# Optimization experiments

Measured on AMD Instinct MI355X. Metric: run time of the kernel, lower is better.

## Reference

```python
import jax, jax.numpy as jnp
import numpy as np

EPS = 1e-5  # BatchNorm eps


def _spmm(x, src, dst, dinv, n):
    # normalized adjacency SpMM: out[d] = dinv[d] * sum_{(s,d) in E} dinv[s] * x[s]
    msg = x[src] * dinv[src][:, None]                      # [E, d]
    agg = jax.ops.segment_sum(msg, dst, num_segments=n)   # [N, d]
    return agg * dinv[:, None]


def _cheb(x, W, b, src, dst, dinv, n):
    # Chebyshev recursion with lambda_max=2: Lhat = -Ahat
    # T0 = X, T1 = Lhat X, Tk = 2 Lhat T_{k-1} - T_{k-2}; out = sum_k T_k W_k + b
    X0 = x
    X1 = -_spmm(x, src, dst, dinv, n)
    out = X0 @ W[0] + X1 @ W[1]
    Xp, Xc = X0, X1
    for k in range(2, W.shape[0]):
        Xn = -2.0 * _spmm(Xc, src, dst, dinv, n) - Xp
        out = out + Xn @ W[k]
        Xp, Xc = Xc, Xn
    return out + b


def _bn(x, gamma, beta):
    # BatchNorm1d over nodes (training-mode batch stats)
    mu = jnp.mean(x, axis=0)
    var = jnp.var(x, axis=0)
    return (x - mu) * jax.lax.rsqrt(var + EPS) * gamma + beta


def setup_inputs() -> dict:
    key = jax.random.key(0)
    ks = jax.random.split(key, 8)
    n, e, fin, h, fout, K = 50000, 800000, 128, 128, 64, 3
    def w(k, shape, fan_in):
        return jax.random.normal(k, shape, jnp.float32) * np.float32(1.0 / np.sqrt(fan_in))
    return {
        "features": jax.random.normal(ks[0], (n, fin), jnp.float32),
        "src": jax.random.randint(ks[1], (e,), 0, n),
        "dst": jax.random.randint(ks[2], (e,), 0, n),
        "W1": w(ks[3], (K, fin, h), K * fin), "b1": jnp.zeros((h,), jnp.float32),
        "W2": w(ks[4], (K, h, h), K * h), "b2": jnp.zeros((h,), jnp.float32),
        "W3": w(ks[5], (K, h, h), K * h), "b3": jnp.zeros((h,), jnp.float32),
        "gamma": jnp.ones((h,), jnp.float32), "beta": jnp.zeros((h,), jnp.float32),
        "mw1": w(ks[6], (h, h), h), "mb1": jnp.zeros((h,), jnp.float32),
        "mw2": w(ks[7], (h, fout), h), "mb2": jnp.zeros((fout,), jnp.float32),
    }


def reference(features, src, dst, W1, b1, W2, b2, W3, b3, gamma, beta, mw1, mb1, mw2, mb2):
    n = features.shape[0]
    deg = jax.ops.segment_sum(jnp.ones(dst.shape, features.dtype), dst, num_segments=n)
    dinv = jax.lax.rsqrt(jnp.maximum(deg, 1.0))
    x = jax.nn.relu(_cheb(features, W1, b1, src, dst, dinv, n))
    x = _bn(x, gamma, beta)
    for _ in range(1, 3):  # self.k = 3 -> cheb2 applied twice (shared weights)
        x = jax.nn.relu(_cheb(x, W2, b2, src, dst, dinv, n))
    x_res = x
    x = jax.nn.relu(_cheb(x, W3, b3, src, dst, dinv, n))
    x = x + x_res  # dropout treated as identity (eval mode)
    return jax.nn.relu(x @ mw1 + mb1) @ mw2 + mb2
```

## Files before the change

kernel.cpp:

```cpp
#include <hip/hip_runtime.h>
#include <hip/hip_bf16.h>

typedef __attribute__((ext_vector_type(4))) float f32x4;
typedef __attribute__((ext_vector_type(8))) short short8;

__device__ inline unsigned short f2bf(float f) {
    union { float f; unsigned int u; } v; v.f = f;
    unsigned int u = v.u;
    return (unsigned short)((u + 0x7fffu + ((u >> 16) & 1u)) >> 16);
}
__device__ inline float bf2f(unsigned short h) {
    union { unsigned int u; float f; } v; v.u = ((unsigned int)h) << 16; return v.f;
}
__device__ inline float bflo(unsigned int p) {
    union { unsigned int u; float f; } v; v.u = p << 16; return v.f;
}
__device__ inline float bfhi(unsigned int p) {
    union { unsigned int u; float f; } v; v.u = p & 0xffff0000u; return v.f;
}
__device__ inline unsigned int packbf(float a, float b) {
    return (unsigned int)f2bf(a) | ((unsigned int)f2bf(b) << 16);
}


__global__ __launch_bounds__(256) void cast_k(const float* __restrict__ x, unsigned short* __restrict__ y, int n4) {
    int i = blockIdx.x * 256 + threadIdx.x;
    if (i >= n4) return;
    f32x4 v = ((const f32x4*)x)[i];
    uint2 o; o.x = packbf(v[0], v[1]); o.y = packbf(v[2], v[3]);
    ((uint2*)y)[i] = o;
}


__global__ __launch_bounds__(256) void deg_count_k(const int* __restrict__ dst, int* __restrict__ deg, int e) {
    int i = blockIdx.x * 256 + threadIdx.x;
    if (i < e) atomicAdd(&deg[dst[i]], 1);
}

__global__ __launch_bounds__(256) void partial_k(const int* __restrict__ deg, int* __restrict__ part, int n) {
    __shared__ int sm[256];
    int t = threadIdx.x;
    int base = blockIdx.x * 1024 + t * 4;
    int s = 0;
#pragma unroll
    for (int j = 0; j < 4; ++j) { int idx = base + j; if (idx < n) s += deg[idx]; }
    sm[t] = s;
    __syncthreads();
    for (int off = 128; off > 0; off >>= 1) {
        if (t < off) sm[t] += sm[t + off];
        __syncthreads();
    }
    if (t == 0) part[blockIdx.x] = sm[0];
}

__global__ __launch_bounds__(256) void scanpart_k(int* __restrict__ part, int nb) {
    __shared__ int sm[256];
    int t = threadIdx.x;
    int v = (t < nb) ? part[t] : 0;
    sm[t] = v;
    __syncthreads();
    for (int off = 1; off < 256; off <<= 1) {
        int u = (t >= off) ? sm[t - off] : 0;
        __syncthreads();
        sm[t] += u;
        __syncthreads();
    }
    if (t < nb) part[t] = sm[t] - v;
}

__global__ __launch_bounds__(256) void rowptr_k(const int* __restrict__ deg, const int* __restrict__ part,
                                                int* __restrict__ rowptr, int* __restrict__ cursor,
                                                float* __restrict__ dinv, int n) {
    __shared__ int sm[256];
    int t = threadIdx.x;
    int base = blockIdx.x * 1024 + t * 4;
    int d[4]; int s = 0;
#pragma unroll
    for (int j = 0; j < 4; ++j) { int idx = base + j; d[j] = (idx < n) ? deg[idx] : 0; s += d[j]; }
    sm[t] = s;
    __syncthreads();
    for (int off = 1; off < 256; off <<= 1) {
        int u = (t >= off) ? sm[t - off] : 0;
        __syncthreads();
        sm[t] += u;
        __syncthreads();
    }
    int ex = part[blockIdx.x] + sm[t] - s;
#pragma unroll
    for (int j = 0; j < 4; ++j) {
        int idx = base + j;
        if (idx < n) {
            rowptr[idx] = ex; cursor[idx] = ex;
            dinv[idx] = rsqrtf(fmaxf((float)d[j], 1.0f));
        }
        ex += d[j];
    }
    if (blockIdx.x == gridDim.x - 1 && t == 255) rowptr[n] = part[blockIdx.x] + sm[255];
}

__global__ __launch_bounds__(256) void scatter_k(const int* __restrict__ src, const int* __restrict__ dst,
                                                 int* __restrict__ cursor, int* __restrict__ csrc, int e) {
    int i = blockIdx.x * 256 + threadIdx.x;
    if (i < e) {
        int p = atomicAdd(&cursor[dst[i]], 1);
        csrc[p] = src[i];
    }
}


__global__ __launch_bounds__(256) void spmm_bf_k(const unsigned short* __restrict__ x, const int* __restrict__ rowptr,
                                                 const int* __restrict__ csrc, const float* __restrict__ dinv,
                                                 unsigned short* __restrict__ out, int n) {
    int lane = threadIdx.x & 63;
    int wave = threadIdx.x >> 6;
    int node = blockIdx.x * 4 + wave;
    if (node >= n) return;
    int g = lane >> 4;
    int c = lane & 15;
    int beg = rowptr[node], end = rowptr[node + 1];
    float acc[8];
#pragma unroll
    for (int j = 0; j < 8; ++j) acc[j] = 0.f;

    int i = beg + g;
    for (; i + 12 < end; i += 16) {
        int s0 = csrc[i], s1 = csrc[i + 4], s2 = csrc[i + 8], s3 = csrc[i + 12];
        float w0 = dinv[s0], w1 = dinv[s1], w2 = dinv[s2], w3 = dinv[s3];
        uint4 v0 = ((const uint4*)(x + (size_t)s0 * 128))[c];
        uint4 v1 = ((const uint4*)(x + (size_t)s1 * 128))[c];
        uint4 v2 = ((const uint4*)(x + (size_t)s2 * 128))[c];
        uint4 v3 = ((const uint4*)(x + (size_t)s3 * 128))[c];
        acc[0] += w0 * bflo(v0.x); acc[1] += w0 * bfhi(v0.x);
        acc[2] += w0 * bflo(v0.y); acc[3] += w0 * bfhi(v0.y);
        acc[4] += w0 * bflo(v0.z); acc[5] += w0 * bfhi(v0.z);
        acc[6] += w0 * bflo(v0.w); acc[7] += w0 * bfhi(v0.w);
        acc[0] += w1 * bflo(v1.x); acc[1] += w1 * bfhi(v1.x);
        acc[2] += w1 * bflo(v1.y); acc[3] += w1 * bfhi(v1.y);
        acc[4] += w1 * bflo(v1.z); acc[5] += w1 * bfhi(v1.z);
        acc[6] += w1 * bflo(v1.w); acc[7] += w1 * bfhi(v1.w);
        acc[0] += w2 * bflo(v2.x); acc[1] += w2 * bfhi(v2.x);
        acc[2] += w2 * bflo(v2.y); acc[3] += w2 * bfhi(v2.y);
        acc[4] += w2 * bflo(v2.z); acc[5] += w2 * bfhi(v2.z);
        acc[6] += w2 * bflo(v2.w); acc[7] += w2 * bfhi(v2.w);
        acc[0] += w3 * bflo(v3.x); acc[1] += w3 * bfhi(v3.x);
        acc[2] += w3 * bflo(v3.y); acc[3] += w3 * bfhi(v3.y);
        acc[4] += w3 * bflo(v3.z); acc[5] += w3 * bfhi(v3.z);
        acc[6] += w3 * bflo(v3.w); acc[7] += w3 * bfhi(v3.w);
    }
    for (; i < end; i += 4) {
        int s0 = csrc[i];
        float w0 = dinv[s0];
        uint4 v0 = ((const uint4*)(x + (size_t)s0 * 128))[c];
        acc[0] += w0 * bflo(v0.x); acc[1] += w0 * bfhi(v0.x);
        acc[2] += w0 * bflo(v0.y); acc[3] += w0 * bfhi(v0.y);
        acc[4] += w0 * bflo(v0.z); acc[5] += w0 * bfhi(v0.z);
        acc[6] += w0 * bflo(v0.w); acc[7] += w0 * bfhi(v0.w);
    }

#pragma unroll
    for (int j = 0; j < 8; ++j) {
        acc[j] += __shfl_xor(acc[j], 16, 64);
        acc[j] += __shfl_xor(acc[j], 32, 64);
    }

    float dd = dinv[node];
    if (g == 0) {
        uint4 o;
        o.x = packbf(acc[0] * dd, acc[1] * dd);
        o.y = packbf(acc[2] * dd, acc[3] * dd);
        o.z = packbf(acc[4] * dd, acc[5] * dd);
        o.w = packbf(acc[6] * dd, acc[7] * dd);
        ((uint4*)(out + (size_t)node * 128))[c] = o;
    }
}


__global__ __launch_bounds__(256) void pack_w_k(const float* __restrict__ W, unsigned short* __restrict__ out,
                                                int K, int N, int cheb) {
    int id = blockIdx.x * 256 + threadIdx.x;
    int total = (K / 32) * (N / 16) * 64;
    if (id >= total) return;
    int lane = id & 63;
    int t2 = id >> 6;
    int nf = N / 16;
    int f = t2 % nf;
    int ks = t2 / nf;
    int col = f * 16 + (lane & 15);
    int kbase = ks * 32 + ((lane >> 4) * 8);
    for (int j = 0; j < 8; ++j) {
        int kg = kbase + j;
        float v;
        if (cheb) {
            int t = kg >> 7, kk = kg & 127;
            const float* W0 = W;
            const float* Wb = W + 16384;
            const float* Wc = W + 32768;
            float w0 = W0[kk * 128 + col], wb = Wb[kk * 128 + col], wc = Wc[kk * 128 + col];
            v = (t == 0) ? (w0 - wc) : (t == 1) ? (-wb) : (2.0f * wc);
        } else {
            v = W[(size_t)kg * N + col];
        }
        out[(size_t)id * 8 + j] = f2bf(v);
    }
}


template<int KSTEPS, int NF, bool RELU, bool RES, bool OUTF32>
__global__ __launch_bounds__(256) void gemm_k(const unsigned short* __restrict__ s0,
                                              const unsigned short* __restrict__ s1,
                                              const unsigned short* __restrict__ s2,
                                              const unsigned short* __restrict__ wp,
                                              const float* __restrict__ bias,
                                              const unsigned short* __restrict__ resid,
                                              void* __restrict__ outv, int n) {
    int lane = threadIdx.x & 63;
    int wave = threadIdx.x >> 6;
    int row0 = blockIdx.x * 64 + wave * 16;
    if (row0 >= n) return;
    int rowA = row0 + (lane & 15);
    if (rowA >= n) rowA = n - 1;
    int kg = (lane >> 4) * 8;

    f32x4 acc[NF];
#pragma unroll
    for (int f = 0; f < NF; ++f) acc[f] = (f32x4)(0.0f);

#pragma unroll
    for (int ks = 0; ks < KSTEPS; ++ks) {
        const unsigned short* sp;
        int kk;
        if (KSTEPS == 12) {
            sp = (ks < 4) ? s0 : ((ks < 8) ? s1 : s2);
            kk = (ks & 3) * 32 + kg;
        } else {
            sp = s0;
            kk = ks * 32 + kg;
        }
        short8 a = *(const short8*)(sp + (size_t)rowA * 128 + kk);
#pragma unroll
        for (int f = 0; f < NF; ++f) {
            short8 b = *(const short8*)(wp + ((size_t)(ks * NF + f) * 512 + lane * 8));
            acc[f] = __builtin_amdgcn_mfma_f32_16x16x32_bf16(a, b, acc[f], 0, 0, 0);
        }
    }

    int colb = lane & 15;
    int rowD = row0 + ((lane >> 4) << 2);
#pragma unroll
    for (int f = 0; f < NF; ++f) {
        int c = f * 16 + colb;
        float bv = bias[c];
#pragma unroll
        for (int r = 0; r < 4; ++r) {
            int row = rowD + r;
            if (row >= n) continue;
            float v = acc[f][r] + bv;
            if (RELU) v = fmaxf(v, 0.0f);
            if (RES) v += bf2f(resid[(size_t)row * 128 + c]);
            if (OUTF32) ((float*)outv)[(size_t)row * (NF * 16) + c] = v;
            else        ((unsigned short*)outv)[(size_t)row * (NF * 16) + c] = f2bf(v);
        }
    }
}


__global__ __launch_bounds__(256) void mlp_fused_k(const unsigned short* __restrict__ x,
                                                   const unsigned short* __restrict__ wp1,
                                                   const float* __restrict__ mb1,
                                                   const unsigned short* __restrict__ wp2,
                                                   const float* __restrict__ mb2,
                                                   float* __restrict__ out, int n) {
    __shared__ unsigned short tlds[64 * 128];
    int lane = threadIdx.x & 63;
    int wave = threadIdx.x >> 6;
    int row0 = blockIdx.x * 64 + wave * 16;
    int rowA = row0 + (lane & 15);
    if (rowA >= n) rowA = n - 1;
    int kg = (lane >> 4) * 8;
    int colb = lane & 15;

    f32x4 acc[8];
#pragma unroll
    for (int f = 0; f < 8; ++f) acc[f] = (f32x4)(0.0f);
#pragma unroll
    for (int ks = 0; ks < 4; ++ks) {
        short8 a = *(const short8*)(x + (size_t)rowA * 128 + ks * 32 + kg);
#pragma unroll
        for (int f = 0; f < 8; ++f) {
            short8 b = *(const short8*)(wp1 + ((size_t)(ks * 8 + f) * 512 + lane * 8));
            acc[f] = __builtin_amdgcn_mfma_f32_16x16x32_bf16(a, b, acc[f], 0, 0, 0);
        }
    }
    int lrowD = wave * 16 + ((lane >> 4) << 2);
#pragma unroll
    for (int f = 0; f < 8; ++f) {
        int c = f * 16 + colb;
        float bv = mb1[c];
#pragma unroll
        for (int r = 0; r < 4; ++r) {
            int lrow = lrowD + r;
            float v = fmaxf(acc[f][r] + bv, 0.0f);
            int byte = lrow * 256 + c * 2;
            byte ^= ((lrow & 7) << 4);
            *(unsigned short*)((char*)tlds + byte) = f2bf(v);
        }
    }
    __syncthreads();

    f32x4 acc2[4];
#pragma unroll
    for (int f = 0; f < 4; ++f) acc2[f] = (f32x4)(0.0f);
    int lrowA = wave * 16 + (lane & 15);
#pragma unroll
    for (int ks = 0; ks < 4; ++ks) {
        int byte = lrowA * 256 + (ks * 32 + kg) * 2;
        byte ^= ((lrowA & 7) << 4);
        short8 a = *(const short8*)((const char*)tlds + byte);
#pragma unroll
        for (int f = 0; f < 4; ++f) {
            short8 b = *(const short8*)(wp2 + ((size_t)(ks * 4 + f) * 512 + lane * 8));
            acc2[f] = __builtin_amdgcn_mfma_f32_16x16x32_bf16(a, b, acc2[f], 0, 0, 0);
        }
    }
    int rowD = row0 + ((lane >> 4) << 2);
#pragma unroll
    for (int f = 0; f < 4; ++f) {
        int c = f * 16 + colb;
        float bv = mb2[c];
#pragma unroll
        for (int r = 0; r < 4; ++r) {
            int row = rowD + r;
            if (row >= n) continue;
            out[(size_t)row * 64 + c] = acc2[f][r] + bv;
        }
    }
}


__global__ __launch_bounds__(256) void bn_stats_k(const unsigned short* __restrict__ x, float* __restrict__ gsum,
                                                  float* __restrict__ gsqs, int n) {
    __shared__ float s1[256], s2[256];
    int c = threadIdx.x & 127;
    int h = threadIdx.x >> 7;
    int r0 = blockIdx.x * 256;
    int rend = r0 + 256; if (rend > n) rend = n;
    float a = 0.f, b = 0.f;
    for (int r = r0 + h; r < rend; r += 2) {
        float v = bf2f(x[(size_t)r * 128 + c]);
        a += v; b += v * v;
    }
    s1[threadIdx.x] = a; s2[threadIdx.x] = b;
    __syncthreads();
    if (threadIdx.x < 128) {
        a = s1[threadIdx.x] + s1[threadIdx.x + 128];
        b = s2[threadIdx.x] + s2[threadIdx.x + 128];
        atomicAdd(&gsum[c], a);
        atomicAdd(&gsqs[c], b);
    }
}

__global__ __launch_bounds__(256) void bn_apply_k(unsigned short* __restrict__ x, const float* __restrict__ gsum,
                                                  const float* __restrict__ gsqs, const float* __restrict__ gamma,
                                                  const float* __restrict__ beta, int n, float inv_n) {
    int i = blockIdx.x * 256 + threadIdx.x;
    if (i >= n * 32) return;
    int c4 = (i & 31) * 4;
    uint2 p = ((uint2*)x)[i];
    float f[4] = { bflo(p.x), bfhi(p.x), bflo(p.y), bfhi(p.y) };
#pragma unroll
    for (int j = 0; j < 4; ++j) {
        int c = c4 + j;
        float mu = gsum[c] * inv_n;
        float var = gsqs[c] * inv_n - mu * mu;
        float sc = rsqrtf(var + 1e-5f) * gamma[c];
        f[j] = (f[j] - mu) * sc + beta[c];
    }
    p.x = packbf(f[0], f[1]);
    p.y = packbf(f[2], f[3]);
    ((uint2*)x)[i] = p;
}


extern "C" void kernel_launch(void* const* d_in, const int* in_sizes, int n_in,
                              void* d_out, int out_size, void* d_ws, size_t ws_size,
                              hipStream_t stream) {
    const float* feat  = (const float*)d_in[0];
    const int*   src   = (const int*)d_in[1];
    const int*   dst   = (const int*)d_in[2];
    const float* W1    = (const float*)d_in[3];
    const float* b1    = (const float*)d_in[4];
    const float* W2    = (const float*)d_in[5];
    const float* b2    = (const float*)d_in[6];
    const float* W3    = (const float*)d_in[7];
    const float* b3    = (const float*)d_in[8];
    const float* gamma = (const float*)d_in[9];
    const float* beta  = (const float*)d_in[10];
    const float* mw1   = (const float*)d_in[11];
    const float* mb1   = (const float*)d_in[12];
    const float* mw2   = (const float*)d_in[13];
    const float* mb2   = (const float*)d_in[14];
    float* outp = (float*)d_out;

    const int n = in_sizes[0] / 128;
    const int e = in_sizes[1];

    char* w = (char*)d_ws;
    auto alloc = [&](size_t bytes) -> void* {
        void* p = (void*)w;
        w += (bytes + 255) & ~(size_t)255;
        return p;
    };
    unsigned short* featb = (unsigned short*)alloc((size_t)n * 128 * 2);
    unsigned short* buf0  = (unsigned short*)alloc((size_t)n * 128 * 2);
    unsigned short* buf1  = (unsigned short*)alloc((size_t)n * 128 * 2);
    unsigned short* buf2  = (unsigned short*)alloc((size_t)n * 128 * 2);
    unsigned short* buf3  = (unsigned short*)alloc((size_t)n * 128 * 2);
    int*   deg    = (int*)alloc((size_t)n * 4);
    float* dinv   = (float*)alloc((size_t)n * 4);
    int*   rowptr = (int*)alloc((size_t)(n + 1) * 4);
    int*   cursor = (int*)alloc((size_t)n * 4);
    int*   csrc   = (int*)alloc((size_t)e * 4);
    int*   part   = (int*)alloc(256 * 4);
    unsigned short* wp1  = (unsigned short*)alloc(12 * 8 * 512 * 2);
    unsigned short* wp2  = (unsigned short*)alloc(12 * 8 * 512 * 2);
    unsigned short* wp3  = (unsigned short*)alloc(12 * 8 * 512 * 2);
    unsigned short* wpm1 = (unsigned short*)alloc(4 * 8 * 512 * 2);
    unsigned short* wpm2 = (unsigned short*)alloc(4 * 4 * 512 * 2);
    float* gsum = (float*)alloc(128 * 4);
    float* gsqs = (float*)alloc(128 * 4);

    const int gE = (e + 255) / 256;
    const int gGemm = (n + 63) / 64;
    const int gSpmm = (n + 3) / 4;
    const int gBnS = (n + 255) / 256;
    const int gBnA = (n * 32 + 255) / 256;
    const int nb = (n + 1023) / 1024;

    cast_k<<<(n * 32 + 255) / 256, 256, 0, stream>>>(feat, featb, n * 32);

    hipMemsetAsync(deg, 0, (size_t)n * 4, stream);
    deg_count_k<<<gE, 256, 0, stream>>>(dst, deg, e);
    partial_k<<<nb, 256, 0, stream>>>(deg, part, n);
    scanpart_k<<<1, 256, 0, stream>>>(part, nb);
    rowptr_k<<<nb, 256, 0, stream>>>(deg, part, rowptr, cursor, dinv, n);
    scatter_k<<<gE, 256, 0, stream>>>(src, dst, cursor, csrc, e);

    pack_w_k<<<(12 * 8 * 64 + 255) / 256, 256, 0, stream>>>(W1, wp1, 384, 128, 1);
    pack_w_k<<<(12 * 8 * 64 + 255) / 256, 256, 0, stream>>>(W2, wp2, 384, 128, 1);
    pack_w_k<<<(12 * 8 * 64 + 255) / 256, 256, 0, stream>>>(W3, wp3, 384, 128, 1);
    pack_w_k<<<(4 * 8 * 64 + 255) / 256, 256, 0, stream>>>(mw1, wpm1, 128, 128, 0);
    pack_w_k<<<(4 * 4 * 64 + 255) / 256, 256, 0, stream>>>(mw2, wpm2, 128, 64, 0);

    spmm_bf_k<<<gSpmm, 256, 0, stream>>>(featb, rowptr, csrc, dinv, buf1, n);
    spmm_bf_k<<<gSpmm, 256, 0, stream>>>(buf1, rowptr, csrc, dinv, buf2, n);
    gemm_k<12, 8, true, false, false><<<gGemm, 256, 0, stream>>>(featb, buf1, buf2, wp1, b1, nullptr, buf0, n);

    hipMemsetAsync(gsum, 0, 128 * 4, stream);
    hipMemsetAsync(gsqs, 0, 128 * 4, stream);
    bn_stats_k<<<gBnS, 256, 0, stream>>>(buf0, gsum, gsqs, n);
    bn_apply_k<<<gBnA, 256, 0, stream>>>(buf0, gsum, gsqs, gamma, beta, n, 1.0f / (float)n);

    spmm_bf_k<<<gSpmm, 256, 0, stream>>>(buf0, rowptr, csrc, dinv, buf1, n);
    spmm_bf_k<<<gSpmm, 256, 0, stream>>>(buf1, rowptr, csrc, dinv, buf2, n);
    gemm_k<12, 8, true, false, false><<<gGemm, 256, 0, stream>>>(buf0, buf1, buf2, wp2, b2, nullptr, buf3, n);

    spmm_bf_k<<<gSpmm, 256, 0, stream>>>(buf3, rowptr, csrc, dinv, buf1, n);
    spmm_bf_k<<<gSpmm, 256, 0, stream>>>(buf1, rowptr, csrc, dinv, buf2, n);
    gemm_k<12, 8, true, false, false><<<gGemm, 256, 0, stream>>>(buf3, buf1, buf2, wp2, b2, nullptr, buf0, n);

    spmm_bf_k<<<gSpmm, 256, 0, stream>>>(buf0, rowptr, csrc, dinv, buf1, n);
    spmm_bf_k<<<gSpmm, 256, 0, stream>>>(buf1, rowptr, csrc, dinv, buf2, n);
    gemm_k<12, 8, true, true, false><<<gGemm, 256, 0, stream>>>(buf0, buf1, buf2, wp3, b3, buf0, buf3, n);

    mlp_fused_k<<<gGemm, 256, 0, stream>>>(buf3, wpm1, mb1, wpm2, mb2, outp, n);
}
```

Before: 540.3 us.

## Fuse BN stats into GEMM, fold BN affine into SpMM, partition atomics by dst range

BatchNorm statistics are now gathered in the first Chebyshev GEMM epilogue through shared-memory atomics, and a tiny kernel turns them into scale and offset. The BN affine is no longer applied in a separate pass. It is folded into the next SpMM, using the sum of neighbour weights for the offset term, and into the GEMM A-operand load for the T0 slice. Degree counting and CSR scatter now split destination nodes into 8 ranges so concurrent atomics land in a smaller address window, at the cost of reading dst 8 times. The five weight-pack launches are merged into one. Together these remove two full passes over the activations and several launches, while adding per-element affine arithmetic in the GEMM inner loop.

```diff
diff --git a/kernel.cpp b/kernel.cpp
--- a/kernel.cpp
+++ b/kernel.cpp
@@ -21,6 +21,8 @@
 __device__ inline unsigned int packbf(float a, float b) {
     return (unsigned int)f2bf(a) | ((unsigned int)f2bf(b) << 16);
 }
+
+#define EPT 4096
 
 
 __global__ __launch_bounds__(256) void cast_k(const float* __restrict__ x, unsigned short* __restrict__ y, int n4) {
@@ -32,9 +34,18 @@
 }
 
 
-__global__ __launch_bounds__(256) void deg_count_k(const int* __restrict__ dst, int* __restrict__ deg, int e) {
-    int i = blockIdx.x * 256 + threadIdx.x;
-    if (i < e) atomicAdd(&deg[dst[i]], 1);
+__global__ __launch_bounds__(256) void deg_count8_k(const int* __restrict__ dst, int* __restrict__ deg,
+                                                    int e, int n, int n8) {
+    int r = blockIdx.x & 7;
+    int chunk = blockIdx.x >> 3;
+    int base = chunk * EPT;
+    int lim = base + EPT; if (lim > e) lim = e;
+    int lo = r * n8;
+    int hi = lo + n8; if (hi > n) hi = n;
+    for (int i = base + threadIdx.x; i < lim; i += 256) {
+        int d = dst[i];
+        if (d >= lo && d < hi) atomicAdd(&deg[d], 1);
+    }
 }
 
 __global__ __launch_bounds__(256) void partial_k(const int* __restrict__ deg, int* __restrict__ part, int n) {
@@ -98,18 +109,29 @@
     if (blockIdx.x == gridDim.x - 1 && t == 255) rowptr[n] = part[blockIdx.x] + sm[255];
 }
 
-__global__ __launch_bounds__(256) void scatter_k(const int* __restrict__ src, const int* __restrict__ dst,
-                                                 int* __restrict__ cursor, int* __restrict__ csrc, int e) {
-    int i = blockIdx.x * 256 + threadIdx.x;
-    if (i < e) {
-        int p = atomicAdd(&cursor[dst[i]], 1);
-        csrc[p] = src[i];
-    }
-}
-
-
+__global__ __launch_bounds__(256) void scatter8_k(const int* __restrict__ src, const int* __restrict__ dst,
+                                                  int* __restrict__ cursor, int* __restrict__ csrc,
+                                                  int e, int n, int n8) {
+    int r = blockIdx.x & 7;
+    int chunk = blockIdx.x >> 3;
+    int base = chunk * EPT;
+    int lim = base + EPT; if (lim > e) lim = e;
+    int lo = r * n8;
+    int hi = lo + n8; if (hi > n) hi = n;
+    for (int i = base + threadIdx.x; i < lim; i += 256) {
+        int d = dst[i];
+        if (d >= lo && d < hi) {
+            int p = atomicAdd(&cursor[d], 1);
+            csrc[p] = src[i];
+        }
+    }
+}
+
+
+template<bool AFF>
 __global__ __launch_bounds__(256) void spmm_bf_k(const unsigned short* __restrict__ x, const int* __restrict__ rowptr,
                                                  const int* __restrict__ csrc, const float* __restrict__ dinv,
+                                                 const float* __restrict__ gscale, const float* __restrict__ goff,
                                                  unsigned short* __restrict__ out, int n) {
     int lane = threadIdx.x & 63;
     int wave = threadIdx.x >> 6;
@@ -119,6 +141,7 @@
     int c = lane & 15;
     int beg = rowptr[node], end = rowptr[node + 1];
     float acc[8];
+    float sw = 0.f;
 #pragma unroll
     for (int j = 0; j < 8; ++j) acc[j] = 0.f;
 
@@ -130,6 +153,7 @@
         uint4 v1 = ((const uint4*)(x + (size_t)s1 * 128))[c];
         uint4 v2 = ((const uint4*)(x + (size_t)s2 * 128))[c];
         uint4 v3 = ((const uint4*)(x + (size_t)s3 * 128))[c];
+        if (AFF) sw += w0 + w1 + w2 + w3;
         acc[0] += w0 * bflo(v0.x); acc[1] += w0 * bfhi(v0.x);
         acc[2] += w0 * bflo(v0.y); acc[3] += w0 * bfhi(v0.y);
         acc[4] += w0 * bflo(v0.z); acc[5] += w0 * bfhi(v0.z);
@@ -151,6 +175,7 @@
         int s0 = csrc[i];
         float w0 = dinv[s0];
         uint4 v0 = ((const uint4*)(x + (size_t)s0 * 128))[c];
+        if (AFF) sw += w0;
         acc[0] += w0 * bflo(v0.x); acc[1] += w0 * bfhi(v0.x);
         acc[2] += w0 * bflo(v0.y); acc[3] += w0 * bfhi(v0.y);
         acc[4] += w0 * bflo(v0.z); acc[5] += w0 * bfhi(v0.z);
@@ -162,9 +187,24 @@
         acc[j] += __shfl_xor(acc[j], 16, 64);
         acc[j] += __shfl_xor(acc[j], 32, 64);
     }
+    if (AFF) {
+        sw += __shfl_xor(sw, 16, 64);
+        sw += __shfl_xor(sw, 32, 64);
+    }
 
     float dd = dinv[node];
     if (g == 0) {
+        if (AFF) {
+            f32x4 sc0 = ((const f32x4*)(gscale + c * 8))[0];
+            f32x4 sc1 = ((const f32x4*)(gscale + c * 8))[1];
+            f32x4 of0 = ((const f32x4*)(goff + c * 8))[0];
+            f32x4 of1 = ((const f32x4*)(goff + c * 8))[1];
+#pragma unroll
+            for (int j = 0; j < 4; ++j) {
+                acc[j] = sc0[j] * acc[j] + of0[j] * sw;
+                acc[4 + j] = sc1[j] * acc[4 + j] + of1[j] * sw;
+            }
+        }
         uint4 o;
         o.x = packbf(acc[0] * dd, acc[1] * dd);
         o.y = packbf(acc[2] * dd, acc[3] * dd);
@@ -175,9 +215,8 @@
 }
 
 
-__global__ __launch_bounds__(256) void pack_w_k(const float* __restrict__ W, unsigned short* __restrict__ out,
-                                                int K, int N, int cheb) {
-    int id = blockIdx.x * 256 + threadIdx.x;
+__device__ inline void pack_one(const float* __restrict__ W, unsigned short* __restrict__ out,
+                                int K, int N, int cheb, int id) {
     int total = (K / 32) * (N / 16) * 64;
     if (id >= total) return;
     int lane = id & 63;
@@ -192,10 +231,7 @@
         float v;
         if (cheb) {
             int t = kg >> 7, kk = kg & 127;
-            const float* W0 = W;
-            const float* Wb = W + 16384;
-            const float* Wc = W + 32768;
-            float w0 = W0[kk * 128 + col], wb = Wb[kk * 128 + col], wc = Wc[kk * 128 + col];
+            float w0 = W[kk * 128 + col], wb = W[16384 + kk * 128 + col], wc = W[32768 + kk * 128 + col];
             v = (t == 0) ? (w0 - wc) : (t == 1) ? (-wb) : (2.0f * wc);
         } else {
             v = W[(size_t)kg * N + col];
@@ -204,61 +240,119 @@
     }
 }
 
-
-template<int KSTEPS, int NF, bool RELU, bool RES, bool OUTF32>
+__global__ __launch_bounds__(256) void pack_all_k(const float* W1, unsigned short* wp1,
+                                                  const float* W2, unsigned short* wp2,
+                                                  const float* W3, unsigned short* wp3,
+                                                  const float* mw1, unsigned short* wpm1,
+                                                  const float* mw2, unsigned short* wpm2) {
+    int b = blockIdx.x, t = threadIdx.x;
+    if (b < 24)       pack_one(W1, wp1, 384, 128, 1, b * 256 + t);
+    else if (b < 48)  pack_one(W2, wp2, 384, 128, 1, (b - 24) * 256 + t);
+    else if (b < 72)  pack_one(W3, wp3, 384, 128, 1, (b - 48) * 256 + t);
+    else if (b < 80)  pack_one(mw1, wpm1, 128, 128, 0, (b - 72) * 256 + t);
+    else              pack_one(mw2, wpm2, 128, 64, 0, (b - 80) * 256 + t);
+}
+
+
+__global__ __launch_bounds__(128) void bn_coef_k(const float* __restrict__ gsum, const float* __restrict__ gsqs,
+                                                 const float* __restrict__ gamma, const float* __restrict__ beta,
+                                                 float* __restrict__ gscale, float* __restrict__ goff, float inv_n) {
+    int c = threadIdx.x;
+    float mu = gsum[c] * inv_n;
+    float var = gsqs[c] * inv_n - mu * mu;
+    float sc = rsqrtf(var + 1e-5f) * gamma[c];
+    gscale[c] = sc;
+    goff[c] = beta[c] - mu * sc;
+}
+
+
+template<int KSTEPS, int NF, bool RELU, bool RES, bool OUTF32, bool STATS, bool AFFA>
 __global__ __launch_bounds__(256) void gemm_k(const unsigned short* __restrict__ s0,
                                               const unsigned short* __restrict__ s1,
                                               const unsigned short* __restrict__ s2,
                                               const unsigned short* __restrict__ wp,
                                               const float* __restrict__ bias,
                                               const unsigned short* __restrict__ resid,
+                                              const float* __restrict__ gscale,
+                                              const float* __restrict__ goff,
+                                              float* __restrict__ gsum, float* __restrict__ gsqs,
                                               void* __restrict__ outv, int n) {
+    __shared__ float bs[128], bq[128];
     int lane = threadIdx.x & 63;
     int wave = threadIdx.x >> 6;
     int row0 = blockIdx.x * 64 + wave * 16;
-    if (row0 >= n) return;
-    int rowA = row0 + (lane & 15);
-    if (rowA >= n) rowA = n - 1;
-    int kg = (lane >> 4) * 8;
-
-    f32x4 acc[NF];
-#pragma unroll
-    for (int f = 0; f < NF; ++f) acc[f] = (f32x4)(0.0f);
-
-#pragma unroll
-    for (int ks = 0; ks < KSTEPS; ++ks) {
-        const unsigned short* sp;
-        int kk;
-        if (KSTEPS == 12) {
-            sp = (ks < 4) ? s0 : ((ks < 8) ? s1 : s2);
-            kk = (ks & 3) * 32 + kg;
-        } else {
-            sp = s0;
-            kk = ks * 32 + kg;
-        }
-        short8 a = *(const short8*)(sp + (size_t)rowA * 128 + kk);
+    bool active = row0 < n;
+    if (!STATS && !active) return;
+
+    if (STATS) {
+        if (threadIdx.x < 128) { bs[threadIdx.x] = 0.f; bq[threadIdx.x] = 0.f; }
+        __syncthreads();
+    }
+
+    if (active) {
+        int rowA = row0 + (lane & 15);
+        if (rowA >= n) rowA = n - 1;
+        int kg = (lane >> 4) * 8;
+
+        f32x4 acc[NF];
+#pragma unroll
+        for (int f = 0; f < NF; ++f) acc[f] = (f32x4)(0.0f);
+
+#pragma unroll
+        for (int ks = 0; ks < KSTEPS; ++ks) {
+            const unsigned short* sp;
+            int kk;
+            if (KSTEPS == 12) {
+                sp = (ks < 4) ? s0 : ((ks < 8) ? s1 : s2);
+                kk = (ks & 3) * 32 + kg;
+            } else {
+                sp = s0;
+                kk = ks * 32 + kg;
+            }
+            short8 a = *(const short8*)(sp + (size_t)rowA * 128 + kk);
+            if (AFFA && ks < 4) {
+                union { unsigned short u[8]; short8 v; } af;
+#pragma unroll
+                for (int j = 0; j < 8; ++j) {
+                    float xv = bf2f((unsigned short)a[j]);
+                    af.u[j] = f2bf(xv * gscale[kk + j] + goff[kk + j]);
+                }
+                a = af.v;
+            }
+#pragma unroll
+            for (int f = 0; f < NF; ++f) {
+                short8 b = *(const short8*)(wp + ((size_t)(ks * NF + f) * 512 + lane * 8));
+                acc[f] = __builtin_amdgcn_mfma_f32_16x16x32_bf16(a, b, acc[f], 0, 0, 0);
+            }
+        }
+
+        int colb = lane & 15;
+        int rowD = row0 + ((lane >> 4) << 2);
 #pragma unroll
         for (int f = 0; f < NF; ++f) {
-            short8 b = *(const short8*)(wp + ((size_t)(ks * NF + f) * 512 + lane * 8));
-            acc[f] = __builtin_amdgcn_mfma_f32_16x16x32_bf16(a, b, acc[f], 0, 0, 0);
-        }
-    }
-
-    int colb = lane & 15;
-    int rowD = row0 + ((lane >> 4) << 2);
-#pragma unroll
-    for (int f = 0; f < NF; ++f) {
-        int c = f * 16 + colb;
-        float bv = bias[c];
-#pragma unroll
-        for (int r = 0; r < 4; ++r) {
-            int row = rowD + r;
-            if (row >= n) continue;
-            float v = acc[f][r] + bv;
-            if (RELU) v = fmaxf(v, 0.0f);
-            if (RES) v += bf2f(resid[(size_t)row * 128 + c]);
-            if (OUTF32) ((float*)outv)[(size_t)row * (NF * 16) + c] = v;
-            else        ((unsigned short*)outv)[(size_t)row * (NF * 16) + c] = f2bf(v);
+            int c = f * 16 + colb;
+            float bv = bias[c];
+            float ls = 0.f, lq = 0.f;
+#pragma unroll
+            for (int r = 0; r < 4; ++r) {
+                int row = rowD + r;
+                if (row >= n) continue;
+                float v = acc[f][r] + bv;
+                if (RELU) v = fmaxf(v, 0.0f);
+                if (RES) v += bf2f(resid[(size_t)row * 128 + c]);
+                if (STATS) { ls += v; lq += v * v; }
+                if (OUTF32) ((float*)outv)[(size_t)row * (NF * 16) + c] = v;
+                else        ((unsigned short*)outv)[(size_t)row * (NF * 16) + c] = f2bf(v);
+            }
+            if (STATS) { atomicAdd(&bs[c], ls); atomicAdd(&bq[c], lq); }
+        }
+    }
+
+    if (STATS) {
+        __syncthreads();
+        if (threadIdx.x < 128) {
+            atomicAdd(&gsum[threadIdx.x], bs[threadIdx.x]);
+            atomicAdd(&gsqs[threadIdx.x], bq[threadIdx.x]);
         }
     }
 }
@@ -334,50 +428,6 @@
             out[(size_t)row * 64 + c] = acc2[f][r] + bv;
         }
     }
-}
-
-
-__global__ __launch_bounds__(256) void bn_stats_k(const unsigned short* __restrict__ x, float* __restrict__ gsum,
-                                                  float* __restrict__ gsqs, int n) {
-    __shared__ float s1[256], s2[256];
-    int c = threadIdx.x & 127;
-    int h = threadIdx.x >> 7;
-    int r0 = blockIdx.x * 256;
-    int rend = r0 + 256; if (rend > n) rend = n;
-    float a = 0.f, b = 0.f;
-    for (int r = r0 + h; r < rend; r += 2) {
-        float v = bf2f(x[(size_t)r * 128 + c]);
-        a += v; b += v * v;
-    }
-    s1[threadIdx.x] = a; s2[threadIdx.x] = b;
-    __syncthreads();
-    if (threadIdx.x < 128) {
-        a = s1[threadIdx.x] + s1[threadIdx.x + 128];
-        b = s2[threadIdx.x] + s2[threadIdx.x + 128];
-        atomicAdd(&gsum[c], a);
-        atomicAdd(&gsqs[c], b);
-    }
-}
-
-__global__ __launch_bounds__(256) void bn_apply_k(unsigned short* __restrict__ x, const float* __restrict__ gsum,
-                                                  const float* __restrict__ gsqs, const float* __restrict__ gamma,
-                                                  const float* __restrict__ beta, int n, float inv_n) {
-    int i = blockIdx.x * 256 + threadIdx.x;
-    if (i >= n * 32) return;
-    int c4 = (i & 31) * 4;
-    uint2 p = ((uint2*)x)[i];
-    float f[4] = { bflo(p.x), bfhi(p.x), bflo(p.y), bfhi(p.y) };
-#pragma unroll
-    for (int j = 0; j < 4; ++j) {
-        int c = c4 + j;
-        float mu = gsum[c] * inv_n;
-        float var = gsqs[c] * inv_n - mu * mu;
-        float sc = rsqrtf(var + 1e-5f) * gamma[c];
-        f[j] = (f[j] - mu) * sc + beta[c];
-    }
-    p.x = packbf(f[0], f[1]);
-    p.y = packbf(f[2], f[3]);
-    ((uint2*)x)[i] = p;
 }
 
 
@@ -403,6 +453,7 @@
 
     const int n = in_sizes[0] / 128;
     const int e = in_sizes[1];
+    const int n8 = (n + 7) / 8;
 
     char* w = (char*)d_ws;
     auto alloc = [&](size_t bytes) -> void* {
@@ -426,51 +477,46 @@
     unsigned short* wp3  = (unsigned short*)alloc(12 * 8 * 512 * 2);
     unsigned short* wpm1 = (unsigned short*)alloc(4 * 8 * 512 * 2);
     unsigned short* wpm2 = (unsigned short*)alloc(4 * 4 * 512 * 2);
-    float* gsum = (float*)alloc(128 * 4);
-    float* gsqs = (float*)alloc(128 * 4);
-
-    const int gE = (e + 255) / 256;
+    float* gsum   = (float*)alloc(128 * 4);
+    float* gsqs   = (float*)alloc(128 * 4);
+    float* gscale = (float*)alloc(128 * 4);
+    float* goff   = (float*)alloc(128 * 4);
+
     const int gGemm = (n + 63) / 64;
     const int gSpmm = (n + 3) / 4;
-    const int gBnS = (n + 255) / 256;
-    const int gBnA = (n * 32 + 255) / 256;
     const int nb = (n + 1023) / 1024;
+    const int gE8 = 8 * ((e + EPT - 1) / EPT);
 
     cast_k<<<(n * 32 + 255) / 256, 256, 0, stream>>>(feat, featb, n * 32);
-
     hipMemsetAsync(deg, 0, (size_t)n * 4, stream);
-    deg_count_k<<<gE, 256, 0, stream>>>(dst, deg, e);
+    hipMemsetAsync(gsum, 0, 1024, stream);
+    deg_count8_k<<<gE8, 256, 0, stream>>>(dst, deg, e, n, n8);
     partial_k<<<nb, 256, 0, stream>>>(deg, part, n);
     scanpart_k<<<1, 256, 0, stream>>>(part, nb);
     rowptr_k<<<nb, 256, 0, stream>>>(deg, part, rowptr, cursor, dinv, n);
-    scatter_k<<<gE, 256, 0, stream>>>(src, dst, cursor, csrc, e);
-
-    pack_w_k<<<(12 * 8 * 64 + 255) / 256, 256, 0, stream>>>(W1, wp1, 384, 128, 1);
-    pack_w_k<<<(12 * 8 * 64 + 255) / 256, 256, 0, stream>>>(W2, wp2, 384, 128, 1);
-    pack_w_k<<<(12 * 8 * 64 + 255) / 256, 256, 0, stream>>>(W3, wp3, 384, 128, 1);
-    pack_w_k<<<(4 * 8 * 64 + 255) / 256, 256, 0, stream>>>(mw1, wpm1, 128, 128, 0);
-    pack_w_k<<<(4 * 4 * 64 + 255) / 256, 256, 0, stream>>>(mw2, wpm2, 128, 64, 0);
-
-    spmm_bf_k<<<gSpmm, 256, 0, stream>>>(featb, rowptr, csrc, dinv, buf1, n);
-    spmm_bf_k<<<gSpmm, 256, 0, stream>>>(buf1, rowptr, csrc, dinv, buf2, n);
-    gemm_k<12, 8, true, false, false><<<gGemm, 256, 0, stream>>>(featb, buf1, buf2, wp1, b1, nullptr, buf0, n);
-
-    hipMemsetAsync(gsum, 0, 128 * 4, stream);
-    hipMemsetAsync(gsqs, 0, 128 * 4, stream);
-    bn_stats_k<<<gBnS, 256, 0, stream>>>(buf0, gsum, gsqs, n);
-    bn_apply_k<<<gBnA, 256, 0, stream>>>(buf0, gsum, gsqs, gamma, beta, n, 1.0f / (float)n);
-
-    spmm_bf_k<<<gSpmm, 256, 0, stream>>>(buf0, rowptr, csrc, dinv, buf1, n);
-    spmm_bf_k<<<gSpmm, 256, 0, stream>>>(buf1, rowptr, csrc, dinv, buf2, n);
-    gemm_k<12, 8, true, false, false><<<gGemm, 256, 0, stream>>>(buf0, buf1, buf2, wp2, b2, nullptr, buf3, n);
-
-    spmm_bf_k<<<gSpmm, 256, 0, stream>>>(buf3, rowptr, csrc, dinv, buf1, n);
-    spmm_bf_k<<<gSpmm, 256, 0, stream>>>(buf1, rowptr, csrc, dinv, buf2, n);
-    gemm_k<12, 8, true, false, false><<<gGemm, 256, 0, stream>>>(buf3, buf1, buf2, wp2, b2, nullptr, buf0, n);
-
-    spmm_bf_k<<<gSpmm, 256, 0, stream>>>(buf0, rowptr, csrc, dinv, buf1, n);
-    spmm_bf_k<<<gSpmm, 256, 0, stream>>>(buf1, rowptr, csrc, dinv, buf2, n);
-    gemm_k<12, 8, true, true, false><<<gGemm, 256, 0, stream>>>(buf0, buf1, buf2, wp3, b3, buf0, buf3, n);
+    scatter8_k<<<gE8, 256, 0, stream>>>(src, dst, cursor, csrc, e, n, n8);
+    pack_all_k<<<84, 256, 0, stream>>>(W1, wp1, W2, wp2, W3, wp3, mw1, wpm1, mw2, wpm2);
+
+    spmm_bf_k<false><<<gSpmm, 256, 0, stream>>>(featb, rowptr, csrc, dinv, nullptr, nullptr, buf1, n);
+    spmm_bf_k<false><<<gSpmm, 256, 0, stream>>>(buf1, rowptr, csrc, dinv, nullptr, nullptr, buf2, n);
+    gemm_k<12, 8, true, false, false, true, false><<<gGemm, 256, 0, stream>>>(
+        featb, buf1, buf2, wp1, b1, nullptr, nullptr, nullptr, gsum, gsqs, buf0, n);
+    bn_coef_k<<<1, 128, 0, stream>>>(gsum, gsqs, gamma, beta, gscale, goff, 1.0f / (float)n);
+
+    spmm_bf_k<true><<<gSpmm, 256, 0, stream>>>(buf0, rowptr, csrc, dinv, gscale, goff, buf1, n);
+    spmm_bf_k<false><<<gSpmm, 256, 0, stream>>>(buf1, rowptr, csrc, dinv, nullptr, nullptr, buf2, n);
+    gemm_k<12, 8, true, false, false, false, true><<<gGemm, 256, 0, stream>>>(
+        buf0, buf1, buf2, wp2, b2, nullptr, gscale, goff, nullptr, nullptr, buf3, n);
+
+    spmm_bf_k<false><<<gSpmm, 256, 0, stream>>>(buf3, rowptr, csrc, dinv, nullptr, nullptr, buf1, n);
+    spmm_bf_k<false><<<gSpmm, 256, 0, stream>>>(buf1, rowptr, csrc, dinv, nullptr, nullptr, buf2, n);
+    gemm_k<12, 8, true, false, false, false, false><<<gGemm, 256, 0, stream>>>(
+        buf3, buf1, buf2, wp2, b2, nullptr, nullptr, nullptr, nullptr, nullptr, buf0, n);
+
+    spmm_bf_k<false><<<gSpmm, 256, 0, stream>>>(buf0, rowptr, csrc, dinv, nullptr, nullptr, buf1, n);
+    spmm_bf_k<false><<<gSpmm, 256, 0, stream>>>(buf1, rowptr, csrc, dinv, nullptr, nullptr, buf2, n);
+    gemm_k<12, 8, true, true, false, false, false><<<gGemm, 256, 0, stream>>>(
+        buf0, buf1, buf2, wp3, b3, buf0, nullptr, nullptr, nullptr, nullptr, buf3, n);
 
     mlp_fused_k<<<gGemm, 256, 0, stream>>>(buf3, wpm1, mb1, wpm2, mb2, outp, n);
 }
```

Result: faster. 497.2 us (-8.0%).
